# Performance work log

Hardware: AMD Instinct MI355X
Metric: run time of the kernel (lower is better)

The kernel has to match this reference:

```python
import jax, jax.numpy as jnp
import numpy as np

N, E, F_IN, HID, C = 50000, 800000, 512, 256, 64
K, ALPHA = 10, 0.1


def setup_inputs() -> dict:
    key = jax.random.key(0)
    ks = jax.random.split(key, 6)
    x = jax.random.normal(ks[0], (N, F_IN), dtype=jnp.float32)
    edge_index = jax.random.randint(ks[1], (2, E), 0, N, dtype=jnp.int64)
    W1 = jax.random.normal(ks[2], (F_IN, HID), dtype=jnp.float32) / np.sqrt(F_IN)
    b1 = jnp.zeros((HID,), dtype=jnp.float32)
    W2 = jax.random.normal(ks[3], (HID, C), dtype=jnp.float32) / np.sqrt(HID)
    b2 = jnp.zeros((C,), dtype=jnp.float32)
    return {"x": x, "W1": W1, "b1": b1, "W2": W2, "b2": b2, "edge_index": edge_index}


def reference(x, W1, b1, W2, b2, edge_index):
    # MLP (dropout is identity in eval mode)
    h = jax.nn.relu(x @ W1 + b1)
    h = h @ W2 + b2  # [N, C]

    n = x.shape[0]
    self_loops = jnp.arange(n, dtype=edge_index.dtype)
    row = jnp.concatenate([edge_index[0], self_loops])  # source nodes
    col = jnp.concatenate([edge_index[1], self_loops])  # target nodes

    # GCN symmetric normalization with self-loops (PyG gcn_norm)
    deg = jax.ops.segment_sum(jnp.ones_like(col, dtype=h.dtype), col, num_segments=n)
    dinv = jnp.where(deg > 0, jax.lax.rsqrt(jnp.maximum(deg, 1e-12)), 0.0)
    norm = (dinv[row] * dinv[col])[:, None]  # [E+N, 1]

    x0 = h

    def step(z, _):
        msg = z[row] * norm                                    # gather + scale
        agg = jax.ops.segment_sum(msg, col, num_segments=n)    # scatter-add
        return (1.0 - ALPHA) * agg + ALPHA * x0, None

    z, _ = jax.lax.scan(step, x0, None, length=K)
    return z
```

## Files before the change

kernel.cpp:

```cpp
#include <hip/hip_runtime.h>

#define N_NODES 50000
#define N_EDGES 800000
#define F_INDIM 512
#define HID     256
#define N_CLS   64
#define K_STEPS 10
#define ALPHA_V 0.1f

#define NPB 28
#define NPW 7
#define ECAP 1536

typedef __attribute__((ext_vector_type(8))) short short8;
typedef __attribute__((ext_vector_type(4))) float f32x4;
typedef __attribute__((ext_vector_type(4))) unsigned short ushort4v;

__device__ __forceinline__ unsigned short f2bf(float f) {
  unsigned u = __builtin_bit_cast(unsigned, f);
  unsigned r = (u + 0x7fffu + ((u >> 16) & 1u)) >> 16;
  return (unsigned short)r;
}
__device__ __forceinline__ float bflo(unsigned g) {
  return __builtin_bit_cast(float, g << 16);
}
__device__ __forceinline__ float bfhi(unsigned g) {
  return __builtin_bit_cast(float, g & 0xffff0000u);
}

#define GLOAD_LDS16(g, l)                                                        \
  __builtin_amdgcn_global_load_lds(                                              \
      (const __attribute__((address_space(1))) unsigned int*)(g),                \
      (__attribute__((address_space(3))) unsigned int*)(l), 16, 0, 0)

__global__ void detect_kernel(const int* __restrict__ eb, int* __restrict__ flag) {
  __shared__ int any;
  if (threadIdx.x == 0) any = 0;
  __syncthreads();
  for (int j = threadIdx.x; j < 1024; j += 256) {
    if (eb[2 * j + 1] != 0) atomicOr(&any, 1);
  }
  __syncthreads();
  if (threadIdx.x == 0) flag[0] = any ? 0 : 1;
}

__global__ void count_kernel(const int* __restrict__ eb, const int* __restrict__ flagp,
                             int* __restrict__ cnt) {
  int e = blockIdx.x * 256 + threadIdx.x;
  if (e >= N_EDGES) return;
  int sh = flagp[0];
  int c = eb[((size_t)(N_EDGES + e)) << sh];
  atomicAdd(&cnt[c], 1);
}

__global__ void scan1_kernel(const int* __restrict__ cnt, int* __restrict__ ptr,
                             int* __restrict__ bsum) {
  __shared__ int sm[256];
  int t = threadIdx.x;
  int i = blockIdx.x * 256 + t;
  int v = (i < N_NODES) ? cnt[i] : 0;
  sm[t] = v;
  __syncthreads();
  for (int off = 1; off < 256; off <<= 1) {
    int x = sm[t];
    if (t >= off) x += sm[t - off];
    __syncthreads();
    sm[t] = x;
    __syncthreads();
  }
  int incl = sm[t];
  if (i < N_NODES) ptr[i] = incl - v;
  if (t == 255) bsum[blockIdx.x] = incl;
}

__global__ void scan2_kernel(int* __restrict__ bsum, int nblk) {
  __shared__ int sm[256];
  int t = threadIdx.x;
  int v = (t < nblk) ? bsum[t] : 0;
  sm[t] = v;
  __syncthreads();
  for (int off = 1; off < 256; off <<= 1) {
    int x = sm[t];
    if (t >= off) x += sm[t - off];
    __syncthreads();
    sm[t] = x;
    __syncthreads();
  }
  int incl = sm[t];
  if (t < nblk) bsum[t] = incl - v;
}

__global__ void scan3_kernel(int* __restrict__ ptr, const int* __restrict__ bsum) {
  int i = blockIdx.x * 256 + threadIdx.x;
  if (i < N_NODES) ptr[i] += bsum[i >> 8];
  if (i == 0) ptr[N_NODES] = N_EDGES;
}

__global__ void dinv_kernel(const int* __restrict__ cnt, const int* __restrict__ ptr,
                            float* __restrict__ dinv, float* __restrict__ selfw,
                            int* __restrict__ cursor) {
  int i = blockIdx.x * 256 + threadIdx.x;
  if (i >= N_NODES) return;
  float di = rsqrtf((float)cnt[i] + 1.0f);
  dinv[i] = di;
  selfw[i] = (1.0f - ALPHA_V) * di * di;
  cursor[i] = ptr[i];
}

__global__ void fill_kernel(const int* __restrict__ eb, const int* __restrict__ flagp,
                            const float* __restrict__ dinv, int* __restrict__ cursor,
                            int2* __restrict__ epack) {
  int e = blockIdx.x * 256 + threadIdx.x;
  if (e >= N_EDGES) return;
  int sh = flagp[0];
  int r = eb[((size_t)e) << sh];
  int c = eb[((size_t)(N_EDGES + e)) << sh];
  int pos = atomicAdd(&cursor[c], 1);
  float w = (1.0f - ALPHA_V) * dinv[r] * dinv[c];
  epack[pos] = make_int2(r, __float_as_int(w));
}

__global__ void prep_w(const float* __restrict__ W1, const float* __restrict__ W2,
                       unsigned short* __restrict__ W1T, unsigned short* __restrict__ W2T) {
  int i = blockIdx.x * 256 + threadIdx.x;
  if (i < F_INDIM * HID) {
    int k = i >> 8, c = i & 255;
    W1T[(size_t)c * F_INDIM + k] = f2bf(W1[i]);
  }
  int j = i - F_INDIM * HID;
  if (j >= 0 && j < HID * N_CLS) {
    int k = j >> 6, c = j & 63;
    W2T[(size_t)c * HID + k] = f2bf(W2[j]);
  }
}

__global__ __launch_bounds__(256, 4) void gemm1_mfma(
    const float* __restrict__ A, const unsigned short* __restrict__ BT,
    const float* __restrict__ bias, unsigned short* __restrict__ H, int M) {
  __shared__ unsigned short Ab[2][128 * 32];
  __shared__ unsigned short Bb[2][128 * 32];
  const int t = threadIdx.x;
  const int wave = t >> 6, lane = t & 63;
  const int wr = wave >> 1, wc = wave & 1;
  const int l15 = lane & 15, l4 = lane >> 4;
  const int row0 = blockIdx.x * 128, col0 = blockIdx.y * 128;

  f32x4 acc[4][4];
#pragma unroll
  for (int m = 0; m < 4; ++m)
#pragma unroll
    for (int n = 0; n < 4; ++n) acc[m][n] = (f32x4)0.0f;

  const int NT = F_INDIM / 32;

  auto stageB = [&](int buf, int kt) {
#pragma unroll
    for (int i = 0; i < 2; ++i) {
      int row = wave * 32 + i * 16 + (lane >> 2);
      int g = lane & 3;
      int kg = g ^ ((row >> 1) & 3);
      const unsigned short* src = BT + (size_t)(col0 + row) * F_INDIM + kt * 32 + kg * 8;
      unsigned short* dst = &Bb[buf][(wave * 32 + i * 16) * 32];
      GLOAD_LDS16(src, dst);
    }
  };
  f32x4 ar[4];
  int arow[4], acol[4];
  auto loadA = [&](int kt) {
#pragma unroll
    for (int i = 0; i < 4; ++i) {
      int idx = (i * 256 + t) * 4;
      int row = idx >> 5;
      int col = idx & 31;
      arow[i] = row; acol[i] = col;
      int gr = row0 + row;
      if (gr > M - 1) gr = M - 1;
      ar[i] = *(const f32x4*)(A + (size_t)gr * F_INDIM + kt * 32 + col);
    }
  };
  auto writeA = [&](int buf) {
#pragma unroll
    for (int i = 0; i < 4; ++i) {
      int row = arow[i], col = acol[i];
      int g = col >> 3;
      int gp = g ^ ((row >> 1) & 3);
      ushort4v o;
#pragma unroll
      for (int j = 0; j < 4; ++j) o[j] = f2bf(ar[i][j]);
      *(ushort4v*)(&Ab[buf][row * 32 + gp * 8 + (col & 7)]) = o;
    }
  };
  auto compute = [&](int buf) {
    short8 af[4], bf[4];
#pragma unroll
    for (int m = 0; m < 4; ++m) {
      int rowA = wr * 64 + m * 16 + l15;
      af[m] = *(const short8*)(&Ab[buf][rowA * 32 + (l4 ^ ((rowA >> 1) & 3)) * 8]);
    }
#pragma unroll
    for (int n = 0; n < 4; ++n) {
      int c = wc * 64 + n * 16 + l15;
      bf[n] = *(const short8*)(&Bb[buf][c * 32 + (l4 ^ ((c >> 1) & 3)) * 8]);
    }
#pragma unroll
    for (int m = 0; m < 4; ++m)
#pragma unroll
      for (int n = 0; n < 4; ++n)
        acc[m][n] = __builtin_amdgcn_mfma_f32_16x16x32_bf16(af[m], bf[n], acc[m][n], 0, 0, 0);
  };

  stageB(0, 0);
  loadA(0);
  writeA(0);
  __syncthreads();
#pragma unroll 4
  for (int kt = 0; kt < NT; ++kt) {
    int cur = kt & 1;
    if (kt + 1 < NT) {
      stageB(cur ^ 1, kt + 1);
      loadA(kt + 1);
    }
    compute(cur);
    if (kt + 1 < NT) writeA(cur ^ 1);
    __syncthreads();
  }

  float bv[4];
#pragma unroll
  for (int n = 0; n < 4; ++n) bv[n] = bias[col0 + wc * 64 + n * 16 + l15];
#pragma unroll
  for (int m = 0; m < 4; ++m)
#pragma unroll
    for (int i = 0; i < 4; ++i) {
      int grow = row0 + wr * 64 + m * 16 + l4 * 4 + i;
      if (grow >= M) continue;
#pragma unroll
      for (int n = 0; n < 4; ++n) {
        int gcol = col0 + wc * 64 + n * 16 + l15;
        float v = fmaxf(acc[m][n][i] + bv[n], 0.0f);
        H[(size_t)grow * HID + gcol] = f2bf(v);
      }
    }
}

__global__ __launch_bounds__(256) void gemm2_mfma(
    const unsigned short* __restrict__ Hm, const unsigned short* __restrict__ BT,
    const float* __restrict__ bias, unsigned short* __restrict__ Ch,
    int roff, int M) {
  const int t = threadIdx.x;
  const int wave = t >> 6, lane = t & 63;
  const int l15 = lane & 15, l4 = lane >> 4;
  const int row0 = blockIdx.x * 64 + wave * 16;

  f32x4 acc[4];
#pragma unroll
  for (int n = 0; n < 4; ++n) acc[n] = (f32x4)0.0f;

  int gr = row0 + l15;
  if (gr > M - 1) gr = M - 1;
  const unsigned short* arow = Hm + (size_t)gr * HID + l4 * 8;

#pragma unroll
  for (int kt = 0; kt < HID / 32; ++kt) {
    short8 af = *(const short8*)(arow + kt * 32);
    short8 bf[4];
#pragma unroll
    for (int n = 0; n < 4; ++n)
      bf[n] = *(const short8*)(BT + (size_t)(n * 16 + l15) * HID + kt * 32 + l4 * 8);
#pragma unroll
    for (int n = 0; n < 4; ++n)
      acc[n] = __builtin_amdgcn_mfma_f32_16x16x32_bf16(af, bf[n], acc[n], 0, 0, 0);
  }

#pragma unroll
  for (int n = 0; n < 4; ++n) {
    int gcol = n * 16 + l15;
    float bv = bias[gcol];
#pragma unroll
    for (int i = 0; i < 4; ++i) {
      int grow = row0 + l4 * 4 + i;
      if (grow < M) {
        float v = acc[n][i] + bv;
        Ch[(size_t)(roff + grow) * N_CLS + gcol] = f2bf(v);
      }
    }
  }
}

template <bool LAST>
__global__ __launch_bounds__(256) void prop_step(
    const unsigned int* __restrict__ zin, const unsigned int* __restrict__ x0h,
    const float* __restrict__ selfw, const int* __restrict__ ptr,
    const int2* __restrict__ epack, unsigned int* __restrict__ zout,
    float* __restrict__ outf) {
  __shared__ int2 erec[ECAP];
  __shared__ int lptr[NPB + 1];
  __shared__ float lsw[NPB];

  const int tid = threadIdx.x;
  const int n0 = blockIdx.x * NPB;
  int nEnd = N_NODES - n0;
  if (nEnd > NPB) nEnd = NPB;

  if (tid <= nEnd) lptr[tid] = ptr[n0 + tid];
  if (tid < nEnd) lsw[tid] = selfw[n0 + tid];
  __syncthreads();
  const int base = lptr[0];
  const int cnt = lptr[nEnd] - base;
  for (int i = tid; i < cnt && i < ECAP; i += 256) erec[i] = epack[base + i];
  __syncthreads();

  const int wv = tid >> 6, lane = tid & 63;
  const int half = lane >> 5, cl = lane & 31;

  auto run = [&](auto getrec) {
    for (int ni = wv * NPW; ni < wv * NPW + NPW; ++ni) {
      if (ni >= nEnd) break;
      const int node = n0 + ni;
      float a0 = 0.0f, a1 = 0.0f;
      if (half == 0) {
        unsigned zs = zin[(size_t)node * 32 + cl];
        unsigned xs = x0h[(size_t)node * 32 + cl];
        float sw = lsw[ni];
        a0 = fmaf(sw, bflo(zs), ALPHA_V * bflo(xs));
        a1 = fmaf(sw, bfhi(zs), ALPHA_V * bfhi(xs));
      }
      int e = lptr[ni] - base, e1 = lptr[ni + 1] - base;
      for (; e + 16 <= e1; e += 16) {
        int2 p[8];
#pragma unroll
        for (int j = 0; j < 8; ++j) p[j] = getrec(e + 2 * j + half);
        unsigned g[8];
#pragma unroll
        for (int j = 0; j < 8; ++j) g[j] = zin[(size_t)p[j].x * 32 + cl];
#pragma unroll
        for (int j = 0; j < 8; ++j) {
          float w = __int_as_float(p[j].y);
          a0 = fmaf(w, bflo(g[j]), a0);
          a1 = fmaf(w, bfhi(g[j]), a1);
        }
      }
      if (e < e1) {
        int2 p[8];
        float m[8];
#pragma unroll
        for (int j = 0; j < 8; ++j) {
          int gi = e + 2 * j + half;
          bool ok = gi < e1;
          p[j] = getrec(ok ? gi : e);
          m[j] = ok ? 1.0f : 0.0f;
        }
        unsigned g[8];
#pragma unroll
        for (int j = 0; j < 8; ++j) g[j] = zin[(size_t)p[j].x * 32 + cl];
#pragma unroll
        for (int j = 0; j < 8; ++j) {
          float w = m[j] * __int_as_float(p[j].y);
          a0 = fmaf(w, bflo(g[j]), a0);
          a1 = fmaf(w, bfhi(g[j]), a1);
        }
      }
      a0 += __shfl_xor(a0, 32);
      a1 += __shfl_xor(a1, 32);
      if (half == 0) {
        if (LAST) {
          *(float2*)(outf + (size_t)node * 64 + 2 * cl) = make_float2(a0, a1);
        } else {
          zout[(size_t)node * 32 + cl] =
              (unsigned)f2bf(a0) | ((unsigned)f2bf(a1) << 16);
        }
      }
    }
  };

  if (cnt <= ECAP) {
    run([&](int i) { return erec[i]; });
  } else {
    run([&](int i) { return epack[base + i]; });
  }
}

extern "C" void kernel_launch(void* const* d_in, const int* in_sizes, int n_in,
                              void* d_out, int out_size, void* d_ws, size_t ws_size,
                              hipStream_t stream) {
  const float* x  = (const float*)d_in[0];
  const float* W1 = (const float*)d_in[1];
  const float* b1 = (const float*)d_in[2];
  const float* W2 = (const float*)d_in[3];
  const float* b2 = (const float*)d_in[4];
  const int*   eb = (const int*)d_in[5];
  float* out = (float*)d_out;

  char* ws = (char*)d_ws;
  size_t off = 0;
  auto alloc = [&](size_t bytes) -> void* {
    void* p = ws + off;
    off = (off + bytes + 255) & ~(size_t)255;
    return p;
  };

  int*   flagp  = (int*)alloc(256);
  int*   cnt    = (int*)alloc(N_NODES * sizeof(int));
  int*   ptr    = (int*)alloc((N_NODES + 1) * sizeof(int));
  int*   cursor = (int*)alloc(N_NODES * sizeof(int));
  int*   bsum   = (int*)alloc(256 * sizeof(int));
  float* dinv   = (float*)alloc(N_NODES * sizeof(float));
  float* selfw  = (float*)alloc(N_NODES * sizeof(float));
  int2*  epack  = (int2*)alloc((size_t)N_EDGES * sizeof(int2));
  unsigned short* W1T = (unsigned short*)alloc((size_t)HID * F_INDIM * sizeof(unsigned short));
  unsigned short* W2T = (unsigned short*)alloc((size_t)N_CLS * HID * sizeof(unsigned short));
  unsigned int* x0h = (unsigned int*)alloc((size_t)N_NODES * 32 * sizeof(unsigned int));
  unsigned int* z1  = (unsigned int*)alloc((size_t)N_NODES * 32 * sizeof(unsigned int));
  unsigned int* z2  = (unsigned int*)alloc((size_t)N_NODES * 32 * sizeof(unsigned int));

  int nchunks = 1;
  while (nchunks < 16) {
    size_t hbytes = (size_t)(N_NODES / nchunks) * HID * sizeof(unsigned short);
    if (off + hbytes <= ws_size) break;
    nchunks <<= 1;
  }
  int Mc = N_NODES / nchunks;
  unsigned short* h = (unsigned short*)alloc((size_t)Mc * HID * sizeof(unsigned short));

  hipMemsetAsync(cnt, 0, N_NODES * sizeof(int), stream);
  detect_kernel<<<1, 256, 0, stream>>>(eb, flagp);
  count_kernel<<<(N_EDGES + 255) / 256, 256, 0, stream>>>(eb, flagp, cnt);
  int nblk = (N_NODES + 255) / 256;
  scan1_kernel<<<nblk, 256, 0, stream>>>(cnt, ptr, bsum);
  scan2_kernel<<<1, 256, 0, stream>>>(bsum, nblk);
  scan3_kernel<<<nblk, 256, 0, stream>>>(ptr, bsum);
  dinv_kernel<<<nblk, 256, 0, stream>>>(cnt, ptr, dinv, selfw, cursor);
  fill_kernel<<<(N_EDGES + 255) / 256, 256, 0, stream>>>(eb, flagp, dinv, cursor, epack);
  prep_w<<<(F_INDIM * HID + HID * N_CLS + 255) / 256, 256, 0, stream>>>(W1, W2, W1T, W2T);

  for (int ci = 0; ci < nchunks; ++ci) {
    const float* Achunk = x + (size_t)ci * Mc * F_INDIM;
    dim3 g1((Mc + 127) / 128, HID / 128);
    gemm1_mfma<<<g1, 256, 0, stream>>>(Achunk, W1T, b1, h, Mc);
    dim3 g2((Mc + 63) / 64, 1);
    gemm2_mfma<<<g2, 256, 0, stream>>>(h, W2T, b2,
        (unsigned short*)x0h, ci * Mc, Mc);
  }

  int pgrid = (N_NODES + NPB - 1) / NPB;
  const unsigned int* zin = x0h;
  unsigned int* zo[2] = {z1, z2};
  for (int s = 0; s < K_STEPS - 1; ++s) {
    unsigned int* zout = zo[s & 1];
    prop_step<false><<<pgrid, 256, 0, stream>>>(zin, x0h, selfw, ptr, epack, zout, nullptr);
    zin = zout;
  }
  prop_step<true><<<pgrid, 256, 0, stream>>>(zin, x0h, selfw, ptr, epack, nullptr, out);
}
```

Measured before the change: 379.9 us.

## Split propagation into two source-half passes and shrink gemm1 row tile

Edges are bucketed by whether the source node falls in the lower or upper half of the node range, giving two CSR segments. Each propagation step becomes two passes, each gathering from only half of z, so the gathered working set is smaller and may stay cache-resident. The first pass writes fp32 partial sums that the second pass reads back. gemm1 also moves to a 64-row tile with one M-fragment per wave to raise block count. The cost is twice the kernel launches, extra partial-sum traffic, and a smaller shared edge cache.

Result: slower. 476.1 us (+25.3%).

```diff
diff --git a/kernel.cpp b/kernel.cpp
--- a/kernel.cpp
+++ b/kernel.cpp
@@ -7,10 +7,12 @@
 #define N_CLS   64
 #define K_STEPS 10
 #define ALPHA_V 0.1f
+#define MID     25000
+#define NS      (2 * N_NODES)
 
 #define NPB 28
 #define NPW 7
-#define ECAP 1536
+#define ECAP 768
 
 typedef __attribute__((ext_vector_type(8))) short short8;
 typedef __attribute__((ext_vector_type(4))) float f32x4;
@@ -45,12 +47,13 @@
 }
 
 __global__ void count_kernel(const int* __restrict__ eb, const int* __restrict__ flagp,
-                             int* __restrict__ cnt) {
+                             int* __restrict__ cnt2) {
   int e = blockIdx.x * 256 + threadIdx.x;
   if (e >= N_EDGES) return;
   int sh = flagp[0];
+  int r = eb[((size_t)e) << sh];
   int c = eb[((size_t)(N_EDGES + e)) << sh];
-  atomicAdd(&cnt[c], 1);
+  atomicAdd(&cnt2[(r >= MID ? N_NODES : 0) + c], 1);
 }
 
 __global__ void scan1_kernel(const int* __restrict__ cnt, int* __restrict__ ptr,
@@ -58,7 +61,7 @@
   __shared__ int sm[256];
   int t = threadIdx.x;
   int i = blockIdx.x * 256 + t;
-  int v = (i < N_NODES) ? cnt[i] : 0;
+  int v = (i < NS) ? cnt[i] : 0;
   sm[t] = v;
   __syncthreads();
   for (int off = 1; off < 256; off <<= 1) {
@@ -69,17 +72,17 @@
     __syncthreads();
   }
   int incl = sm[t];
-  if (i < N_NODES) ptr[i] = incl - v;
+  if (i < NS) ptr[i] = incl - v;
   if (t == 255) bsum[blockIdx.x] = incl;
 }
 
 __global__ void scan2_kernel(int* __restrict__ bsum, int nblk) {
-  __shared__ int sm[256];
+  __shared__ int sm[512];
   int t = threadIdx.x;
   int v = (t < nblk) ? bsum[t] : 0;
   sm[t] = v;
   __syncthreads();
-  for (int off = 1; off < 256; off <<= 1) {
+  for (int off = 1; off < 512; off <<= 1) {
     int x = sm[t];
     if (t >= off) x += sm[t - off];
     __syncthreads();
@@ -90,21 +93,25 @@
   if (t < nblk) bsum[t] = incl - v;
 }
 
-__global__ void scan3_kernel(int* __restrict__ ptr, const int* __restrict__ bsum) {
+__global__ void scan3_kernel(int* __restrict__ ptr, const int* __restrict__ bsum,
+                             int* __restrict__ cursor) {
   int i = blockIdx.x * 256 + threadIdx.x;
-  if (i < N_NODES) ptr[i] += bsum[i >> 8];
-  if (i == 0) ptr[N_NODES] = N_EDGES;
-}
-
-__global__ void dinv_kernel(const int* __restrict__ cnt, const int* __restrict__ ptr,
-                            float* __restrict__ dinv, float* __restrict__ selfw,
-                            int* __restrict__ cursor) {
+  if (i < NS) {
+    int v = ptr[i] + bsum[i >> 8];
+    ptr[i] = v;
+    cursor[i] = v;
+  }
+  if (i == 0) ptr[NS] = N_EDGES;
+}
+
+__global__ void dinv_kernel(const int* __restrict__ cnt2, float* __restrict__ dinv,
+                            float* __restrict__ selfw) {
   int i = blockIdx.x * 256 + threadIdx.x;
   if (i >= N_NODES) return;
-  float di = rsqrtf((float)cnt[i] + 1.0f);
+  float deg = (float)(cnt2[i] + cnt2[N_NODES + i]);
+  float di = rsqrtf(deg + 1.0f);
   dinv[i] = di;
   selfw[i] = (1.0f - ALPHA_V) * di * di;
-  cursor[i] = ptr[i];
 }
 
 __global__ void fill_kernel(const int* __restrict__ eb, const int* __restrict__ flagp,
@@ -115,7 +122,7 @@
   int sh = flagp[0];
   int r = eb[((size_t)e) << sh];
   int c = eb[((size_t)(N_EDGES + e)) << sh];
-  int pos = atomicAdd(&cursor[c], 1);
+  int pos = atomicAdd(&cursor[(r >= MID ? N_NODES : 0) + c], 1);
   float w = (1.0f - ALPHA_V) * dinv[r] * dinv[c];
   epack[pos] = make_int2(r, __float_as_int(w));
 }
@@ -137,19 +144,16 @@
 __global__ __launch_bounds__(256, 4) void gemm1_mfma(
     const float* __restrict__ A, const unsigned short* __restrict__ BT,
     const float* __restrict__ bias, unsigned short* __restrict__ H, int M) {
-  __shared__ unsigned short Ab[2][128 * 32];
+  __shared__ unsigned short Ab[2][64 * 32];
   __shared__ unsigned short Bb[2][128 * 32];
   const int t = threadIdx.x;
   const int wave = t >> 6, lane = t & 63;
-  const int wr = wave >> 1, wc = wave & 1;
   const int l15 = lane & 15, l4 = lane >> 4;
-  const int row0 = blockIdx.x * 128, col0 = blockIdx.y * 128;
-
-  f32x4 acc[4][4];
-#pragma unroll
-  for (int m = 0; m < 4; ++m)
-#pragma unroll
-    for (int n = 0; n < 4; ++n) acc[m][n] = (f32x4)0.0f;
+  const int row0 = blockIdx.x * 64, col0 = blockIdx.y * 128;
+
+  f32x4 acc[8];
+#pragma unroll
+  for (int n = 0; n < 8; ++n) acc[n] = (f32x4)0.0f;
 
   const int NT = F_INDIM / 32;
 
@@ -164,12 +168,12 @@
       GLOAD_LDS16(src, dst);
     }
   };
-  f32x4 ar[4];
-  int arow[4], acol[4];
+  f32x4 ar[2];
+  int arow[2], acol[2];
   auto loadA = [&](int kt) {
 #pragma unroll
-    for (int i = 0; i < 4; ++i) {
-      int idx = (i * 256 + t) * 4;
+    for (int i = 0; i < 2; ++i) {
+      int idx = wave * 512 + i * 256 + lane * 4;
       int row = idx >> 5;
       int col = idx & 31;
       arow[i] = row; acol[i] = col;
@@ -180,7 +184,7 @@
   };
   auto writeA = [&](int buf) {
 #pragma unroll
-    for (int i = 0; i < 4; ++i) {
+    for (int i = 0; i < 2; ++i) {
       int row = arow[i], col = acol[i];
       int g = col >> 3;
       int gp = g ^ ((row >> 1) & 3);
@@ -191,22 +195,17 @@
     }
   };
   auto compute = [&](int buf) {
-    short8 af[4], bf[4];
-#pragma unroll
-    for (int m = 0; m < 4; ++m) {
-      int rowA = wr * 64 + m * 16 + l15;
-      af[m] = *(const short8*)(&Ab[buf][rowA * 32 + (l4 ^ ((rowA >> 1) & 3)) * 8]);
-    }
-#pragma unroll
-    for (int n = 0; n < 4; ++n) {
-      int c = wc * 64 + n * 16 + l15;
+    int rowA = wave * 16 + l15;
+    short8 af = *(const short8*)(&Ab[buf][rowA * 32 + (l4 ^ ((rowA >> 1) & 3)) * 8]);
+    short8 bf[8];
+#pragma unroll
+    for (int n = 0; n < 8; ++n) {
+      int c = n * 16 + l15;
       bf[n] = *(const short8*)(&Bb[buf][c * 32 + (l4 ^ ((c >> 1) & 3)) * 8]);
     }
 #pragma unroll
-    for (int m = 0; m < 4; ++m)
-#pragma unroll
-      for (int n = 0; n < 4; ++n)
-        acc[m][n] = __builtin_amdgcn_mfma_f32_16x16x32_bf16(af[m], bf[n], acc[m][n], 0, 0, 0);
+    for (int n = 0; n < 8; ++n)
+      acc[n] = __builtin_amdgcn_mfma_f32_16x16x32_bf16(af, bf[n], acc[n], 0, 0, 0);
   };
 
   stageB(0, 0);
@@ -225,22 +224,20 @@
     __syncthreads();
   }
 
-  float bv[4];
-#pragma unroll
-  for (int n = 0; n < 4; ++n) bv[n] = bias[col0 + wc * 64 + n * 16 + l15];
-#pragma unroll
-  for (int m = 0; m < 4; ++m)
-#pragma unroll
-    for (int i = 0; i < 4; ++i) {
-      int grow = row0 + wr * 64 + m * 16 + l4 * 4 + i;
-      if (grow >= M) continue;
-#pragma unroll
-      for (int n = 0; n < 4; ++n) {
-        int gcol = col0 + wc * 64 + n * 16 + l15;
-        float v = fmaxf(acc[m][n][i] + bv[n], 0.0f);
-        H[(size_t)grow * HID + gcol] = f2bf(v);
-      }
-    }
+  float bv[8];
+#pragma unroll
+  for (int n = 0; n < 8; ++n) bv[n] = bias[col0 + n * 16 + l15];
+#pragma unroll
+  for (int i = 0; i < 4; ++i) {
+    int grow = row0 + wave * 16 + l4 * 4 + i;
+    if (grow >= M) continue;
+#pragma unroll
+    for (int n = 0; n < 8; ++n) {
+      int gcol = col0 + n * 16 + l15;
+      float v = fmaxf(acc[n][i] + bv[n], 0.0f);
+      H[(size_t)grow * HID + gcol] = f2bf(v);
+    }
+  }
 }
 
 __global__ __launch_bounds__(256) void gemm2_mfma(
@@ -287,12 +284,12 @@
   }
 }
 
-template <bool LAST>
-__global__ __launch_bounds__(256) void prop_step(
+template <int PHASE>
+__global__ __launch_bounds__(256) void prop_pass(
     const unsigned int* __restrict__ zin, const unsigned int* __restrict__ x0h,
-    const float* __restrict__ selfw, const int* __restrict__ ptr,
-    const int2* __restrict__ epack, unsigned int* __restrict__ zout,
-    float* __restrict__ outf) {
+    const float* __restrict__ selfw, const int* __restrict__ ptr2,
+    const int2* __restrict__ epack, float* __restrict__ zpart,
+    unsigned int* __restrict__ zout, float* __restrict__ outf) {
   __shared__ int2 erec[ECAP];
   __shared__ int lptr[NPB + 1];
   __shared__ float lsw[NPB];
@@ -301,9 +298,10 @@
   const int n0 = blockIdx.x * NPB;
   int nEnd = N_NODES - n0;
   if (nEnd > NPB) nEnd = NPB;
-
-  if (tid <= nEnd) lptr[tid] = ptr[n0 + tid];
-  if (tid < nEnd) lsw[tid] = selfw[n0 + tid];
+  const int HOFF = (PHASE == 0) ? 0 : N_NODES;
+
+  if (tid <= nEnd) lptr[tid] = ptr2[HOFF + n0 + tid];
+  if (PHASE != 0 && tid < nEnd) lsw[tid] = selfw[n0 + tid];
   __syncthreads();
   const int base = lptr[0];
   const int cnt = lptr[nEnd] - base;
@@ -318,12 +316,13 @@
       if (ni >= nEnd) break;
       const int node = n0 + ni;
       float a0 = 0.0f, a1 = 0.0f;
-      if (half == 0) {
+      if (PHASE != 0 && half == 0) {
+        float2 zp = *(const float2*)(zpart + (size_t)node * 64 + 2 * cl);
         unsigned zs = zin[(size_t)node * 32 + cl];
         unsigned xs = x0h[(size_t)node * 32 + cl];
         float sw = lsw[ni];
-        a0 = fmaf(sw, bflo(zs), ALPHA_V * bflo(xs));
-        a1 = fmaf(sw, bfhi(zs), ALPHA_V * bfhi(xs));
+        a0 = zp.x + fmaf(sw, bflo(zs), ALPHA_V * bflo(xs));
+        a1 = zp.y + fmaf(sw, bfhi(zs), ALPHA_V * bfhi(xs));
       }
       int e = lptr[ni] - base, e1 = lptr[ni + 1] - base;
       for (; e + 16 <= e1; e += 16) {
@@ -363,11 +362,13 @@
       a0 += __shfl_xor(a0, 32);
       a1 += __shfl_xor(a1, 32);
       if (half == 0) {
-        if (LAST) {
-          *(float2*)(outf + (size_t)node * 64 + 2 * cl) = make_float2(a0, a1);
-        } else {
+        if (PHASE == 0) {
+          *(float2*)(zpart + (size_t)node * 64 + 2 * cl) = make_float2(a0, a1);
+        } else if (PHASE == 1) {
           zout[(size_t)node * 32 + cl] =
               (unsigned)f2bf(a0) | ((unsigned)f2bf(a1) << 16);
+        } else {
+          *(float2*)(outf + (size_t)node * 64 + 2 * cl) = make_float2(a0, a1);
         }
       }
     }
@@ -400,10 +401,10 @@
   };
 
   int*   flagp  = (int*)alloc(256);
-  int*   cnt    = (int*)alloc(N_NODES * sizeof(int));
-  int*   ptr    = (int*)alloc((N_NODES + 1) * sizeof(int));
-  int*   cursor = (int*)alloc(N_NODES * sizeof(int));
-  int*   bsum   = (int*)alloc(256 * sizeof(int));
+  int*   cnt2   = (int*)alloc(NS * sizeof(int));
+  int*   ptr2   = (int*)alloc((NS + 1) * sizeof(int));
+  int*   cursor = (int*)alloc(NS * sizeof(int));
+  int*   bsum   = (int*)alloc(512 * sizeof(int));
   float* dinv   = (float*)alloc(N_NODES * sizeof(float));
   float* selfw  = (float*)alloc(N_NODES * sizeof(float));
   int2*  epack  = (int2*)alloc((size_t)N_EDGES * sizeof(int2));
@@ -412,6 +413,7 @@
   unsigned int* x0h = (unsigned int*)alloc((size_t)N_NODES * 32 * sizeof(unsigned int));
   unsigned int* z1  = (unsigned int*)alloc((size_t)N_NODES * 32 * sizeof(unsigned int));
   unsigned int* z2  = (unsigned int*)alloc((size_t)N_NODES * 32 * sizeof(unsigned int));
+  float* zpart = (float*)alloc((size_t)N_NODES * N_CLS * sizeof(float));
 
   int nchunks = 1;
   while (nchunks < 16) {
@@ -422,20 +424,20 @@
   int Mc = N_NODES / nchunks;
   unsigned short* h = (unsigned short*)alloc((size_t)Mc * HID * sizeof(unsigned short));
 
-  hipMemsetAsync(cnt, 0, N_NODES * sizeof(int), stream);
+  hipMemsetAsync(cnt2, 0, NS * sizeof(int), stream);
   detect_kernel<<<1, 256, 0, stream>>>(eb, flagp);
-  count_kernel<<<(N_EDGES + 255) / 256, 256, 0, stream>>>(eb, flagp, cnt);
-  int nblk = (N_NODES + 255) / 256;
-  scan1_kernel<<<nblk, 256, 0, stream>>>(cnt, ptr, bsum);
-  scan2_kernel<<<1, 256, 0, stream>>>(bsum, nblk);
-  scan3_kernel<<<nblk, 256, 0, stream>>>(ptr, bsum);
-  dinv_kernel<<<nblk, 256, 0, stream>>>(cnt, ptr, dinv, selfw, cursor);
+  count_kernel<<<(N_EDGES + 255) / 256, 256, 0, stream>>>(eb, flagp, cnt2);
+  int nblk2 = (NS + 255) / 256;
+  scan1_kernel<<<nblk2, 256, 0, stream>>>(cnt2, ptr2, bsum);
+  scan2_kernel<<<1, 512, 0, stream>>>(bsum, nblk2);
+  scan3_kernel<<<nblk2, 256, 0, stream>>>(ptr2, bsum, cursor);
+  dinv_kernel<<<(N_NODES + 255) / 256, 256, 0, stream>>>(cnt2, dinv, selfw);
   fill_kernel<<<(N_EDGES + 255) / 256, 256, 0, stream>>>(eb, flagp, dinv, cursor, epack);
   prep_w<<<(F_INDIM * HID + HID * N_CLS + 255) / 256, 256, 0, stream>>>(W1, W2, W1T, W2T);
 
   for (int ci = 0; ci < nchunks; ++ci) {
     const float* Achunk = x + (size_t)ci * Mc * F_INDIM;
-    dim3 g1((Mc + 127) / 128, HID / 128);
+    dim3 g1((Mc + 63) / 64, HID / 128);
     gemm1_mfma<<<g1, 256, 0, stream>>>(Achunk, W1T, b1, h, Mc);
     dim3 g2((Mc + 63) / 64, 1);
     gemm2_mfma<<<g2, 256, 0, stream>>>(h, W2T, b2,
@@ -445,10 +447,17 @@
   int pgrid = (N_NODES + NPB - 1) / NPB;
   const unsigned int* zin = x0h;
   unsigned int* zo[2] = {z1, z2};
-  for (int s = 0; s < K_STEPS - 1; ++s) {
-    unsigned int* zout = zo[s & 1];
-    prop_step<false><<<pgrid, 256, 0, stream>>>(zin, x0h, selfw, ptr, epack, zout, nullptr);
-    zin = zout;
-  }
-  prop_step<true><<<pgrid, 256, 0, stream>>>(zin, x0h, selfw, ptr, epack, nullptr, out);
-}
+  for (int s = 0; s < K_STEPS; ++s) {
+    prop_pass<0><<<pgrid, 256, 0, stream>>>(zin, x0h, selfw, ptr2, epack,
+                                            zpart, nullptr, nullptr);
+    if (s < K_STEPS - 1) {
+      unsigned int* zout = zo[s & 1];
+      prop_pass<1><<<pgrid, 256, 0, stream>>>(zin, x0h, selfw, ptr2, epack,
+                                              zpart, zout, nullptr);
+      zin = zout;
+    } else {
+      prop_pass<2><<<pgrid, 256, 0, stream>>>(zin, x0h, selfw, ptr2, epack,
+                                              zpart, nullptr, out);
+    }
+  }
+}
```

## Retile gemm1 to 64-row by full-width blocks so x is read once

Applied to the files above, without the earlier changes.

Changes the first GEMM from 128x128 tiles on a 2D grid to 64-row tiles covering all 256 hidden columns, with each wave owning 16 rows and 16 MFMA column tiles. This means each fp32 row of x is loaded and converted to bf16 only once instead of twice, cutting the dominant global read traffic of x. In exchange each block stages the whole W1T k-slice into a larger B buffer, and per-wave data reuse drops because one A fragment now feeds 16 MFMAs with 16 separate B LDS reads. Register pressure and LDS footprint also change, which may affect occupancy.

New measurement: 383.8 us. No clear change (+1.0%).

```diff
diff --git a/kernel.cpp b/kernel.cpp
--- a/kernel.cpp
+++ b/kernel.cpp
@@ -137,39 +137,36 @@
 __global__ __launch_bounds__(256, 4) void gemm1_mfma(
     const float* __restrict__ A, const unsigned short* __restrict__ BT,
     const float* __restrict__ bias, unsigned short* __restrict__ H, int M) {
-  __shared__ unsigned short Ab[2][128 * 32];
-  __shared__ unsigned short Bb[2][128 * 32];
+  __shared__ unsigned short Ab[2][64 * 32];
+  __shared__ unsigned short Bb[2][256 * 32];
   const int t = threadIdx.x;
   const int wave = t >> 6, lane = t & 63;
-  const int wr = wave >> 1, wc = wave & 1;
   const int l15 = lane & 15, l4 = lane >> 4;
-  const int row0 = blockIdx.x * 128, col0 = blockIdx.y * 128;
-
-  f32x4 acc[4][4];
-#pragma unroll
-  for (int m = 0; m < 4; ++m)
-#pragma unroll
-    for (int n = 0; n < 4; ++n) acc[m][n] = (f32x4)0.0f;
+  const int row0 = blockIdx.x * 64;
+
+  f32x4 acc[16];
+#pragma unroll
+  for (int n = 0; n < 16; ++n) acc[n] = (f32x4)0.0f;
 
   const int NT = F_INDIM / 32;
 
   auto stageB = [&](int buf, int kt) {
 #pragma unroll
-    for (int i = 0; i < 2; ++i) {
-      int row = wave * 32 + i * 16 + (lane >> 2);
+    for (int i = 0; i < 4; ++i) {
+      int row = wave * 64 + i * 16 + (lane >> 2);
       int g = lane & 3;
       int kg = g ^ ((row >> 1) & 3);
-      const unsigned short* src = BT + (size_t)(col0 + row) * F_INDIM + kt * 32 + kg * 8;
-      unsigned short* dst = &Bb[buf][(wave * 32 + i * 16) * 32];
+      const unsigned short* src = BT + (size_t)row * F_INDIM + kt * 32 + kg * 8;
+      unsigned short* dst = &Bb[buf][(wave * 64 + i * 16) * 32];
       GLOAD_LDS16(src, dst);
     }
   };
-  f32x4 ar[4];
-  int arow[4], acol[4];
+  f32x4 ar[2];
+  int arow[2], acol[2];
   auto loadA = [&](int kt) {
 #pragma unroll
-    for (int i = 0; i < 4; ++i) {
-      int idx = (i * 256 + t) * 4;
+    for (int i = 0; i < 2; ++i) {
+      int idx = wave * 512 + i * 256 + lane * 4;
       int row = idx >> 5;
       int col = idx & 31;
       arow[i] = row; acol[i] = col;
@@ -180,7 +177,7 @@
   };
   auto writeA = [&](int buf) {
 #pragma unroll
-    for (int i = 0; i < 4; ++i) {
+    for (int i = 0; i < 2; ++i) {
       int row = arow[i], col = acol[i];
       int g = col >> 3;
       int gp = g ^ ((row >> 1) & 3);
@@ -191,22 +188,14 @@
     }
   };
   auto compute = [&](int buf) {
-    short8 af[4], bf[4];
-#pragma unroll
-    for (int m = 0; m < 4; ++m) {
-      int rowA = wr * 64 + m * 16 + l15;
-      af[m] = *(const short8*)(&Ab[buf][rowA * 32 + (l4 ^ ((rowA >> 1) & 3)) * 8]);
-    }
-#pragma unroll
-    for (int n = 0; n < 4; ++n) {
-      int c = wc * 64 + n * 16 + l15;
-      bf[n] = *(const short8*)(&Bb[buf][c * 32 + (l4 ^ ((c >> 1) & 3)) * 8]);
-    }
-#pragma unroll
-    for (int m = 0; m < 4; ++m)
-#pragma unroll
-      for (int n = 0; n < 4; ++n)
-        acc[m][n] = __builtin_amdgcn_mfma_f32_16x16x32_bf16(af[m], bf[n], acc[m][n], 0, 0, 0);
+    int rowA = wave * 16 + l15;
+    short8 af = *(const short8*)(&Ab[buf][rowA * 32 + (l4 ^ ((rowA >> 1) & 3)) * 8]);
+#pragma unroll
+    for (int n = 0; n < 16; ++n) {
+      int c = n * 16 + l15;
+      short8 bf = *(const short8*)(&Bb[buf][c * 32 + (l4 ^ ((c >> 1) & 3)) * 8]);
+      acc[n] = __builtin_amdgcn_mfma_f32_16x16x32_bf16(af, bf, acc[n], 0, 0, 0);
+    }
   };
 
   stageB(0, 0);
@@ -225,22 +214,17 @@
     __syncthreads();
   }
 
-  float bv[4];
-#pragma unroll
-  for (int n = 0; n < 4; ++n) bv[n] = bias[col0 + wc * 64 + n * 16 + l15];
-#pragma unroll
-  for (int m = 0; m < 4; ++m)
-#pragma unroll
-    for (int i = 0; i < 4; ++i) {
-      int grow = row0 + wr * 64 + m * 16 + l4 * 4 + i;
-      if (grow >= M) continue;
-#pragma unroll
-      for (int n = 0; n < 4; ++n) {
-        int gcol = col0 + wc * 64 + n * 16 + l15;
-        float v = fmaxf(acc[m][n][i] + bv[n], 0.0f);
-        H[(size_t)grow * HID + gcol] = f2bf(v);
-      }
-    }
+#pragma unroll
+  for (int i = 0; i < 4; ++i) {
+    int grow = row0 + wave * 16 + l4 * 4 + i;
+    if (grow >= M) continue;
+#pragma unroll
+    for (int n = 0; n < 16; ++n) {
+      int gcol = n * 16 + l15;
+      float v = fmaxf(acc[n][i] + bias[gcol], 0.0f);
+      H[(size_t)grow * HID + gcol] = f2bf(v);
+    }
+  }
 }
 
 __global__ __launch_bounds__(256) void gemm2_mfma(
@@ -435,9 +419,9 @@
 
   for (int ci = 0; ci < nchunks; ++ci) {
     const float* Achunk = x + (size_t)ci * Mc * F_INDIM;
-    dim3 g1((Mc + 127) / 128, HID / 128);
+    dim3 g1((Mc + 63) / 64);
     gemm1_mfma<<<g1, 256, 0, stream>>>(Achunk, W1T, b1, h, Mc);
-    dim3 g2((Mc + 63) / 64, 1);
+    dim3 g2((Mc + 63) / 64);
     gemm2_mfma<<<g2, 256, 0, stream>>>(h, W2T, b2,
         (unsigned short*)x0h, ci * Mc, Mc);
   }
```
